# Optimization experiments

Hardware: AMD Instinct MI355X
Metric: run time of the kernel (lower is better)

Reference implementation:

```python
import jax, jax.numpy as jnp
import numpy as np

D_HEAD = 64
D_MODEL = 1024
N_HEADS = D_MODEL // D_HEAD
MAX_TOKENS = 2048


def setup_inputs() -> dict:
    key = jax.random.key(0)
    ks = jax.random.split(key, 5)
    batch, pos = 2, 2048
    # kaiming_normal_ on (n_heads, d_model, d_head): fan_in = d_model*d_head -> std = sqrt(2/fan_in)
    std_qkv = np.sqrt(2.0 / (D_MODEL * D_HEAD)).astype(np.float32)
    # xavier_normal_ on (d_model, d_model): std = sqrt(2/(fan_in+fan_out))
    std_out = np.sqrt(2.0 / (D_MODEL + D_MODEL)).astype(np.float32)
    return {
        "residual_stream": jax.random.normal(ks[0], (batch, pos, D_MODEL), dtype=jnp.float32),
        "weight_query": jax.random.normal(ks[1], (N_HEADS, D_MODEL, D_HEAD), dtype=jnp.float32) * std_qkv,
        "weight_key": jax.random.normal(ks[2], (N_HEADS, D_MODEL, D_HEAD), dtype=jnp.float32) * std_qkv,
        "weight_value": jax.random.normal(ks[3], (N_HEADS, D_MODEL, D_HEAD), dtype=jnp.float32) * std_qkv,
        "weight_out": jax.random.normal(ks[4], (D_MODEL, D_MODEL), dtype=jnp.float32) * std_out,
    }


def reference(residual_stream, weight_query, weight_key, weight_value, weight_out):
    # QKV projections: [b, p, m] x [h, m, d] -> [b, h, p, d]
    q = jnp.einsum('bpm,hmd->bhpd', residual_stream, weight_query)
    k = jnp.einsum('bpm,hmd->bhpd', residual_stream, weight_key)
    v = jnp.einsum('bpm,hmd->bhpd', residual_stream, weight_value)

    n_tokens = residual_stream.shape[1]
    # scaled scores [b, h, dest, src]
    scores = jnp.einsum('bhqd,bhkd->bhqk', q, k) / jnp.sqrt(jnp.float32(D_HEAD))
    # causal mask: -inf above the diagonal
    causal = jnp.tril(jnp.ones((n_tokens, n_tokens), dtype=bool))
    scores = jnp.where(causal, scores, jnp.float32(-jnp.inf))
    pattern = jax.nn.softmax(scores, axis=-1)

    attn = jnp.einsum('bhqk,bhkd->bhqd', pattern, v)  # [b, h, dest, d_head]
    # concat heads -> [b, p, h*d_head]
    b, h, p, d = attn.shape
    attn_concat = jnp.transpose(attn, (0, 2, 1, 3)).reshape(b, p, h * d)
    return jnp.einsum('bpm,mn->bpn', attn_concat, weight_out)
```

## Files before the change

### kernel.cpp

```cpp
#include <hip/hip_runtime.h>
#include <hip/hip_bf16.h>
#include <stdint.h>


typedef __bf16 bf16x8 __attribute__((ext_vector_type(8)));
typedef float f32x4 __attribute__((ext_vector_type(4)));
typedef unsigned short u16;

__device__ __forceinline__ u16 f2bf(float f) {
  unsigned u = __float_as_uint(f);
  u += 0x7fffu + ((u >> 16) & 1u);
  return (u16)(u >> 16);
}

__global__ __launch_bounds__(256) void xcvt_k(const float* __restrict__ in,
                                              u16* __restrict__ out) {
  int i = (blockIdx.x * 256 + threadIdx.x) * 8;
  float4 f0 = *reinterpret_cast<const float4*>(in + i);
  float4 f1 = *reinterpret_cast<const float4*>(in + i + 4);
  u16 tmp[8] = {f2bf(f0.x), f2bf(f0.y), f2bf(f0.z), f2bf(f0.w),
                f2bf(f1.x), f2bf(f1.y), f2bf(f1.z), f2bf(f1.w)};
  *reinterpret_cast<uint4*>(out + i) = *reinterpret_cast<uint4*>(tmp);
}

__global__ __launch_bounds__(256) void transpose_cvt_k(const float* __restrict__ in,
                                                       u16* __restrict__ out,
                                                       int R, int C) {
  __shared__ u16 tile[64][80];
  int b = blockIdx.z;
  int r0 = blockIdx.x * 64, c0 = blockIdx.y * 64;
  const float* ip = in + (size_t)b * R * C;
  u16* op = out + (size_t)b * R * C;
  int t = threadIdx.x;
  int r = t >> 2, cb = (t & 3) * 16;
  const float4* src = reinterpret_cast<const float4*>(ip + (size_t)(r0 + r) * C + c0 + cb);
  u16 tmp[16];
#pragma unroll
  for (int v = 0; v < 4; v++) {
    float4 f = src[v];
    tmp[v * 4 + 0] = f2bf(f.x);
    tmp[v * 4 + 1] = f2bf(f.y);
    tmp[v * 4 + 2] = f2bf(f.z);
    tmp[v * 4 + 3] = f2bf(f.w);
  }
  *reinterpret_cast<uint4*>(&tile[r][cb]) = *reinterpret_cast<uint4*>(&tmp[0]);
  *reinterpret_cast<uint4*>(&tile[r][cb + 8]) = *reinterpret_cast<uint4*>(&tmp[8]);
  __syncthreads();
  int c = t >> 2, rb = (t & 3) * 16;
  uint4 outv[2];
  u16* tp = reinterpret_cast<u16*>(outv);
#pragma unroll
  for (int j = 0; j < 16; j++) tp[j] = tile[rb + j][c];
  uint4* dst = reinterpret_cast<uint4*>(op + (size_t)(c0 + c) * R + r0 + rb);
  dst[0] = outv[0];
  dst[1] = outv[1];
}

__global__ __launch_bounds__(256) void transpose_qkv_k(const float* __restrict__ Wq,
                                                       const float* __restrict__ Wk,
                                                       const float* __restrict__ Wv,
                                                       u16* __restrict__ outBase) {
  __shared__ u16 tile[64][80];
  int z = blockIdx.z;
  int sel = z >> 4, head = z & 15;
  const float* W = (sel == 0) ? Wq : (sel == 1 ? Wk : Wv);
  const float* ip = W + (size_t)head * 65536;
  u16* op = outBase + (size_t)sel * 1048576 + (size_t)head * 65536;
  int r0 = blockIdx.x * 64;
  int t = threadIdx.x;
  int r = t >> 2, cb = (t & 3) * 16;
  const float4* src = reinterpret_cast<const float4*>(ip + (size_t)(r0 + r) * 64 + cb);
  u16 tmp[16];
#pragma unroll
  for (int v = 0; v < 4; v++) {
    float4 f = src[v];
    tmp[v * 4 + 0] = f2bf(f.x);
    tmp[v * 4 + 1] = f2bf(f.y);
    tmp[v * 4 + 2] = f2bf(f.z);
    tmp[v * 4 + 3] = f2bf(f.w);
  }
  *reinterpret_cast<uint4*>(&tile[r][cb]) = *reinterpret_cast<uint4*>(&tmp[0]);
  *reinterpret_cast<uint4*>(&tile[r][cb + 8]) = *reinterpret_cast<uint4*>(&tmp[8]);
  __syncthreads();
  int c = t >> 2, rb = (t & 3) * 16;
  uint4 outv[2];
  u16* tp = reinterpret_cast<u16*>(outv);
#pragma unroll
  for (int j = 0; j < 16; j++) tp[j] = tile[rb + j][c];
  uint4* dst = reinterpret_cast<uint4*>(op + (size_t)c * 1024 + r0 + rb);
  dst[0] = outv[0];
  dst[1] = outv[1];
}

__device__ __forceinline__ void gload16(const u16* g, u16* l) {
  __builtin_amdgcn_global_load_lds(
      (__attribute__((address_space(1))) void*)(g),
      (__attribute__((address_space(3))) void*)(l), 16, 0, 0);
}

__device__ __forceinline__ void gemm128_core(const u16* __restrict__ A,
                                             const u16* __restrict__ BT,
                                             int m0, int n0,
                                             f32x4 (&acc)[4][4]) {
  __shared__ __align__(16) u16 As[2][128][64];
  __shared__ __align__(16) u16 Bs[2][128][64];
  int t = threadIdx.x, l = t & 63;
  int w = t >> 6, wm = w & 1, wn = w >> 1;
  int l15 = l & 15, q4 = l >> 4;
  int r8 = l >> 3;
  int cs = ((l & 7) ^ r8) * 8;
  int swz = l15 & 7;
  int srow = w * 32 + r8;
  const u16* ga = A + (size_t)(m0 + srow) * 1024 + cs;
  const u16* gb = BT + (size_t)(n0 + srow) * 1024 + cs;
  f32x4 z4 = {0.f, 0.f, 0.f, 0.f};
#pragma unroll
  for (int mi = 0; mi < 4; mi++)
#pragma unroll
    for (int nt = 0; nt < 4; nt++) acc[mi][nt] = z4;

#pragma unroll
  for (int i = 0; i < 4; i++) {
    gload16(ga + (size_t)(i * 8) * 1024, &As[0][w * 32 + i * 8][0]);
    gload16(gb + (size_t)(i * 8) * 1024, &Bs[0][w * 32 + i * 8][0]);
  }
  __syncthreads();

  for (int step = 0; step < 16; step++) {
    int cur = step & 1;
    if (step < 15) {
      int k0 = (step + 1) * 64;
#pragma unroll
      for (int i = 0; i < 4; i++) {
        gload16(ga + (size_t)(i * 8) * 1024 + k0, &As[cur ^ 1][w * 32 + i * 8][0]);
        gload16(gb + (size_t)(i * 8) * 1024 + k0, &Bs[cur ^ 1][w * 32 + i * 8][0]);
      }
    }
#pragma unroll
    for (int kk = 0; kk < 2; kk++) {
      bf16x8 af[4], bfr[4];
#pragma unroll
      for (int mi = 0; mi < 4; mi++)
        af[mi] = *reinterpret_cast<const bf16x8*>(
            &As[cur][wm * 64 + mi * 16 + l15][((kk * 4 + q4) ^ swz) * 8]);
#pragma unroll
      for (int nt = 0; nt < 4; nt++)
        bfr[nt] = *reinterpret_cast<const bf16x8*>(
            &Bs[cur][wn * 64 + nt * 16 + l15][((kk * 4 + q4) ^ swz) * 8]);
#pragma unroll
      for (int mi = 0; mi < 4; mi++)
#pragma unroll
        for (int nt = 0; nt < 4; nt++)
          acc[mi][nt] = __builtin_amdgcn_mfma_f32_16x16x32_bf16(af[mi], bfr[nt], acc[mi][nt], 0, 0, 0);
    }
    __syncthreads();
  }
}

__global__ __launch_bounds__(256) void qkv_gemm128_k(const u16* __restrict__ A,
                                                     const u16* __restrict__ BT,
                                                     u16* __restrict__ Q,
                                                     u16* __restrict__ K,
                                                     u16* __restrict__ VT2) {
  const float QSCALE = 0.125f * 1.44269504088896340736f;
  int m0 = blockIdx.x * 128, n0 = blockIdx.y * 128;
  f32x4 acc[4][4];
  gemm128_core(A, BT, m0, n0, acc);
  int t = threadIdx.x, l = t & 63;
  int w = t >> 6, wm = w & 1, wn = w >> 1;
  int l15 = l & 15, q4 = l >> 4;
#pragma unroll
  for (int mi = 0; mi < 4; mi++) {
#pragma unroll
    for (int nt = 0; nt < 4; nt++) {
#pragma unroll
      for (int r = 0; r < 4; r++) {
        int m = m0 + wm * 64 + mi * 16 + q4 * 4 + r;
        int n = n0 + wn * 64 + nt * 16 + l15;
        int wsel = n >> 10, h = (n >> 6) & 15, d = n & 63;
        int b = m >> 11, p = m & 2047;
        size_t bh = (size_t)(b * 16 + h);
        float v = acc[mi][nt][r];
        if (wsel == 0)
          Q[(bh * 2048 + p) * 64 + d] = f2bf(v * QSCALE);
        else if (wsel == 1)
          K[(bh * 2048 + p) * 64 + d] = f2bf(v);
        else
          VT2[((bh * 32 + (p >> 6)) * 64 + d) * 64 + (p & 63)] = f2bf(v);
      }
    }
  }
}

__global__ __launch_bounds__(256) void out_gemm128_k(const u16* __restrict__ A,
                                                     const u16* __restrict__ BT,
                                                     float* __restrict__ O) {
  int m0 = blockIdx.x * 128, n0 = blockIdx.y * 128;
  f32x4 acc[4][4];
  gemm128_core(A, BT, m0, n0, acc);
  int t = threadIdx.x, l = t & 63;
  int w = t >> 6, wm = w & 1, wn = w >> 1;
  int l15 = l & 15, q4 = l >> 4;
#pragma unroll
  for (int mi = 0; mi < 4; mi++) {
#pragma unroll
    for (int nt = 0; nt < 4; nt++) {
#pragma unroll
      for (int r = 0; r < 4; r++) {
        int m = m0 + wm * 64 + mi * 16 + q4 * 4 + r;
        int n = n0 + wn * 64 + nt * 16 + l15;
        O[(size_t)m * 1024 + n] = acc[mi][nt][r];
      }
    }
  }
}

__global__ __launch_bounds__(256) void attn_k(const u16* __restrict__ Q,
                                              const u16* __restrict__ K,
                                              const u16* __restrict__ VT2,
                                              u16* __restrict__ A) {
  __shared__ __align__(16) u16 Ks[2][64][64];
  __shared__ __align__(16) u16 Vs[2][64][64];
  __shared__ u16 P[4][32][72];
  int pr = blockIdx.x, h = blockIdx.y, b = blockIdx.z;
  int qt = b ? (15 - pr) : pr;
  size_t bh = (size_t)(b * 16 + h);
  const u16* Qp = Q + bh * 2048 * 64;
  const u16* Kp = K + bh * 2048 * 64;
  const u16* Vt = VT2 + bh * 32 * 64 * 64;
  int t = threadIdx.x, l = t & 63, w = t >> 6;
  int l15 = l & 15, q4 = l >> 4;
  int r8 = l >> 3, cs = ((l & 7) ^ r8) * 8;
  int swz = l15 & 7;
  const float NEG = -1e30f;
  f32x4 z4 = {0.f, 0.f, 0.f, 0.f};
  int nkt = 2 * qt + 2;
  const u16* kbase = Kp + (size_t)(w * 16 + r8) * 64 + cs;
  const u16* vbase = Vt + (size_t)(w * 16 + r8) * 64 + cs;

  int qr0 = qt * 128 + w * 32;
  bf16x8 qf[2][2];
#pragma unroll
  for (int mi = 0; mi < 2; mi++) {
    const u16* qp = Qp + (size_t)(qr0 + mi * 16 + l15) * 64;
    qf[mi][0] = *reinterpret_cast<const bf16x8*>(qp + q4 * 8);
    qf[mi][1] = *reinterpret_cast<const bf16x8*>(qp + 32 + q4 * 8);
  }
  f32x4 accO[2][4];
  float rs[2][4];
#pragma unroll
  for (int mi = 0; mi < 2; mi++) {
#pragma unroll
    for (int nt = 0; nt < 4; nt++) accO[mi][nt] = z4;
#pragma unroll
    for (int r = 0; r < 4; r++) rs[mi][r] = 0.f;
  }

#pragma unroll
  for (int j = 0; j < 2; j++) {
    gload16(kbase + (size_t)(j * 512), &Ks[0][w * 16 + j * 8][0]);
    gload16(vbase + (size_t)(j * 512), &Vs[0][w * 16 + j * 8][0]);
  }
  __syncthreads();

  for (int kt = 0; kt < nkt; kt++) {
    int cur = kt & 1;
    if (kt < nkt - 1) {
      size_t off = (size_t)(kt + 1) * 4096;
#pragma unroll
      for (int j = 0; j < 2; j++) {
        gload16(kbase + off + j * 512, &Ks[cur ^ 1][w * 16 + j * 8][0]);
        gload16(vbase + off + j * 512, &Vs[cur ^ 1][w * 16 + j * 8][0]);
      }
    }

    f32x4 s[2][4];
#pragma unroll
    for (int mi = 0; mi < 2; mi++)
#pragma unroll
      for (int nt = 0; nt < 4; nt++) s[mi][nt] = z4;
    __builtin_amdgcn_s_setprio(1);
#pragma unroll
    for (int kk = 0; kk < 2; kk++) {
      bf16x8 kf[4];
#pragma unroll
      for (int nt = 0; nt < 4; nt++)
        kf[nt] = *reinterpret_cast<const bf16x8*>(
            &Ks[cur][nt * 16 + l15][((kk * 4 + q4) ^ swz) * 8]);
#pragma unroll
      for (int mi = 0; mi < 2; mi++)
#pragma unroll
        for (int nt = 0; nt < 4; nt++)
          s[mi][nt] = __builtin_amdgcn_mfma_f32_16x16x32_bf16(qf[mi][kk], kf[nt], s[mi][nt], 0, 0, 0);
    }
    __builtin_amdgcn_s_setprio(0);
    if (kt >= 2 * qt) {
      int colbase = (kt - 2 * qt) * 64;
      int rowl = w * 32 + q4 * 4;
#pragma unroll
      for (int mi = 0; mi < 2; mi++)
#pragma unroll
        for (int nt = 0; nt < 4; nt++)
#pragma unroll
          for (int r = 0; r < 4; r++)
            if (colbase + nt * 16 + l15 > rowl + mi * 16 + r) s[mi][nt][r] = NEG;
    }
#pragma unroll
    for (int mi = 0; mi < 2; mi++)
#pragma unroll
      for (int nt = 0; nt < 4; nt++)
#pragma unroll
        for (int r = 0; r < 4; r++) {
          float p = exp2f(s[mi][nt][r]);
          rs[mi][r] += p;
          P[w][mi * 16 + q4 * 4 + r][nt * 16 + l15] = f2bf(p);
        }
    __builtin_amdgcn_s_setprio(1);
#pragma unroll
    for (int kk = 0; kk < 2; kk++) {
      bf16x8 pa[2];
#pragma unroll
      for (int mi = 0; mi < 2; mi++)
        pa[mi] = *reinterpret_cast<const bf16x8*>(&P[w][mi * 16 + l15][kk * 32 + q4 * 8]);
#pragma unroll
      for (int nt = 0; nt < 4; nt++) {
        bf16x8 vf = *reinterpret_cast<const bf16x8*>(
            &Vs[cur][nt * 16 + l15][((kk * 4 + q4) ^ swz) * 8]);
#pragma unroll
        for (int mi = 0; mi < 2; mi++)
          accO[mi][nt] = __builtin_amdgcn_mfma_f32_16x16x32_bf16(pa[mi], vf, accO[mi][nt], 0, 0, 0);
      }
    }
    __builtin_amdgcn_s_setprio(0);
    __syncthreads();
  }

#pragma unroll
  for (int mi = 0; mi < 2; mi++)
#pragma unroll
    for (int r = 0; r < 4; r++) {
      float v = rs[mi][r];
#pragma unroll
      for (int sh = 1; sh < 16; sh <<= 1) v += __shfl_xor(v, sh, 64);
      float inv = 1.f / v;
      int prow = qt * 128 + w * 32 + mi * 16 + q4 * 4 + r;
      size_t base = ((size_t)(b * 2048 + prow)) * 1024 + h * 64;
#pragma unroll
      for (int nt = 0; nt < 4; nt++) A[base + nt * 16 + l15] = f2bf(accO[mi][nt][r] * inv);
    }
}

extern "C" void kernel_launch(void* const* d_in, const int* in_sizes, int n_in,
                              void* d_out, int out_size, void* d_ws, size_t ws_size,
                              hipStream_t stream) {
  const float* X  = (const float*)d_in[0];
  const float* Wq = (const float*)d_in[1];
  const float* Wk = (const float*)d_in[2];
  const float* Wv = (const float*)d_in[3];
  const float* Wo = (const float*)d_in[4];
  float* out = (float*)d_out;

  u16* ws = (u16*)d_ws;
  u16* WqT = ws;
  u16* WoT = WqT + 3145728;
  u16* Xb  = WoT + 1048576;
  u16* Qb  = Xb + 4194304;
  u16* Kb  = Qb + 4194304;
  u16* VT2 = Kb + 4194304;
  u16* Ab  = Xb;

  xcvt_k<<<dim3(2048), 256, 0, stream>>>(X, Xb);
  transpose_qkv_k<<<dim3(16, 1, 48), 256, 0, stream>>>(Wq, Wk, Wv, WqT);
  transpose_cvt_k<<<dim3(16, 16, 1), 256, 0, stream>>>(Wo, WoT, 1024, 1024);

  qkv_gemm128_k<<<dim3(32, 24), 256, 0, stream>>>(Xb, WqT, Qb, Kb, VT2);
  attn_k<<<dim3(16, 16, 2), 256, 0, stream>>>(Qb, Kb, VT2, Ab);
  out_gemm128_k<<<dim3(32, 8), 256, 0, stream>>>(Ab, WoT, out);
}
```

Measured before the change: 228.0 us.

## Switch attention to 32x32x16 MFMA with transposed scores and register-resident P

Rewrites the attention kernel to use 32x32x16 bf16 MFMA tiles, computing S^T (K as A operand, Q as B) so each lane owns one query row. The probabilities are packed to bf16 in registers with v_cvt_pk_bf16_f32 and redistributed across lane halves with v_permlane32_swap, which removes the per-wave P shared-memory staging and its LDS round trip. The row-sum reduction is simplified to one shuffle plus a small LDS buffer at the end. This relies on gfx950-specific instructions and the exact MFMA register layout; any layout mismatch would give wrong results.

```diff
diff --git a/kernel.cpp b/kernel.cpp
--- a/kernel.cpp
+++ b/kernel.cpp
@@ -5,12 +5,23 @@
 
 typedef __bf16 bf16x8 __attribute__((ext_vector_type(8)));
 typedef float f32x4 __attribute__((ext_vector_type(4)));
+typedef float f32x16 __attribute__((ext_vector_type(16)));
 typedef unsigned short u16;
 
 __device__ __forceinline__ u16 f2bf(float f) {
   unsigned u = __float_as_uint(f);
   u += 0x7fffu + ((u >> 16) & 1u);
   return (u16)(u >> 16);
+}
+
+__device__ __forceinline__ uint32_t cvtpk(float lo, float hi) {
+  uint32_t r;
+  asm("v_cvt_pk_bf16_f32 %0, %1, %2" : "=v"(r) : "v"(lo), "v"(hi));
+  return r;
+}
+
+__device__ __forceinline__ void pl32swap(uint32_t& a, uint32_t& b) {
+  asm volatile("v_permlane32_swap_b32 %0, %1" : "+v"(a), "+v"(b));
 }
 
 __global__ __launch_bounds__(256) void xcvt_k(const float* __restrict__ in,
@@ -221,7 +232,7 @@
                                               u16* __restrict__ A) {
   __shared__ __align__(16) u16 Ks[2][64][64];
   __shared__ __align__(16) u16 Vs[2][64][64];
-  __shared__ u16 P[4][32][72];
+  __shared__ float rsbuf[4][32];
   int pr = blockIdx.x, h = blockIdx.y, b = blockIdx.z;
   int qt = b ? (15 - pr) : pr;
   size_t bh = (size_t)(b * 16 + h);
@@ -229,32 +240,26 @@
   const u16* Kp = K + bh * 2048 * 64;
   const u16* Vt = VT2 + bh * 32 * 64 * 64;
   int t = threadIdx.x, l = t & 63, w = t >> 6;
-  int l15 = l & 15, q4 = l >> 4;
+  int l31 = l & 31, hi = l >> 5;
   int r8 = l >> 3, cs = ((l & 7) ^ r8) * 8;
-  int swz = l15 & 7;
+  int swz = l31 & 7;
   const float NEG = -1e30f;
-  f32x4 z4 = {0.f, 0.f, 0.f, 0.f};
   int nkt = 2 * qt + 2;
   const u16* kbase = Kp + (size_t)(w * 16 + r8) * 64 + cs;
   const u16* vbase = Vt + (size_t)(w * 16 + r8) * 64 + cs;
-
-  int qr0 = qt * 128 + w * 32;
-  bf16x8 qf[2][2];
-#pragma unroll
-  for (int mi = 0; mi < 2; mi++) {
-    const u16* qp = Qp + (size_t)(qr0 + mi * 16 + l15) * 64;
-    qf[mi][0] = *reinterpret_cast<const bf16x8*>(qp + q4 * 8);
-    qf[mi][1] = *reinterpret_cast<const bf16x8*>(qp + 32 + q4 * 8);
-  }
-  f32x4 accO[2][4];
-  float rs[2][4];
-#pragma unroll
-  for (int mi = 0; mi < 2; mi++) {
-#pragma unroll
-    for (int nt = 0; nt < 4; nt++) accO[mi][nt] = z4;
-#pragma unroll
-    for (int r = 0; r < 4; r++) rs[mi][r] = 0.f;
-  }
+  int qrow = qt * 128 + w * 32 + l31;
+
+  bf16x8 qb[4];
+#pragma unroll
+  for (int kc = 0; kc < 4; kc++)
+    qb[kc] = *reinterpret_cast<const bf16x8*>(Qp + (size_t)qrow * 64 + kc * 16 + hi * 8);
+
+  f32x16 accO[2];
+#pragma unroll
+  for (int dh = 0; dh < 2; dh++)
+#pragma unroll
+    for (int r = 0; r < 16; r++) accO[dh][r] = 0.f;
+  float rs = 0.f;
 
 #pragma unroll
   for (int j = 0; j < 2; j++) {
@@ -274,80 +279,83 @@
       }
     }
 
-    f32x4 s[2][4];
-#pragma unroll
-    for (int mi = 0; mi < 2; mi++)
-#pragma unroll
-      for (int nt = 0; nt < 4; nt++) s[mi][nt] = z4;
+    f32x16 st[2];
+#pragma unroll
+    for (int kvh = 0; kvh < 2; kvh++)
+#pragma unroll
+      for (int r = 0; r < 16; r++) st[kvh][r] = 0.f;
     __builtin_amdgcn_s_setprio(1);
 #pragma unroll
-    for (int kk = 0; kk < 2; kk++) {
-      bf16x8 kf[4];
-#pragma unroll
-      for (int nt = 0; nt < 4; nt++)
-        kf[nt] = *reinterpret_cast<const bf16x8*>(
-            &Ks[cur][nt * 16 + l15][((kk * 4 + q4) ^ swz) * 8]);
-#pragma unroll
-      for (int mi = 0; mi < 2; mi++)
-#pragma unroll
-        for (int nt = 0; nt < 4; nt++)
-          s[mi][nt] = __builtin_amdgcn_mfma_f32_16x16x32_bf16(qf[mi][kk], kf[nt], s[mi][nt], 0, 0, 0);
+    for (int kc = 0; kc < 4; kc++) {
+      bf16x8 ka0 = *reinterpret_cast<const bf16x8*>(
+          &Ks[cur][l31][((2 * kc + hi) ^ swz) * 8]);
+      bf16x8 ka1 = *reinterpret_cast<const bf16x8*>(
+          &Ks[cur][32 + l31][((2 * kc + hi) ^ swz) * 8]);
+      st[0] = __builtin_amdgcn_mfma_f32_32x32x16_bf16(ka0, qb[kc], st[0], 0, 0, 0);
+      st[1] = __builtin_amdgcn_mfma_f32_32x32x16_bf16(ka1, qb[kc], st[1], 0, 0, 0);
     }
     __builtin_amdgcn_s_setprio(0);
+
     if (kt >= 2 * qt) {
-      int colbase = (kt - 2 * qt) * 64;
-      int rowl = w * 32 + q4 * 4;
-#pragma unroll
-      for (int mi = 0; mi < 2; mi++)
-#pragma unroll
-        for (int nt = 0; nt < 4; nt++)
-#pragma unroll
-          for (int r = 0; r < 4; r++)
-            if (colbase + nt * 16 + l15 > rowl + mi * 16 + r) s[mi][nt][r] = NEG;
-    }
-#pragma unroll
-    for (int mi = 0; mi < 2; mi++)
-#pragma unroll
-      for (int nt = 0; nt < 4; nt++)
-#pragma unroll
-        for (int r = 0; r < 4; r++) {
-          float p = exp2f(s[mi][nt][r]);
-          rs[mi][r] += p;
-          P[w][mi * 16 + q4 * 4 + r][nt * 16 + l15] = f2bf(p);
+      int kvb = kt * 64;
+#pragma unroll
+      for (int kvh = 0; kvh < 2; kvh++)
+#pragma unroll
+        for (int r = 0; r < 16; r++) {
+          int kv = kvb + kvh * 32 + (r & 3) + 8 * (r >> 2) + 4 * hi;
+          if (kv > qrow) st[kvh][r] = NEG;
         }
+    }
+
+#pragma unroll
+    for (int kvh = 0; kvh < 2; kvh++)
+#pragma unroll
+      for (int r = 0; r < 16; r++) {
+        float p = exp2f(st[kvh][r]);
+        st[kvh][r] = p;
+        rs += p;
+      }
+
+    bf16x8 pa[4];
+#pragma unroll
+    for (int ks = 0; ks < 4; ks++) {
+      const f32x16& pp = st[ks >> 1];
+      const int s8 = (ks & 1) * 8;
+      uint32_t x0 = cvtpk(pp[s8 + 0], pp[s8 + 1]);
+      uint32_t x1 = cvtpk(pp[s8 + 2], pp[s8 + 3]);
+      uint32_t y0 = cvtpk(pp[s8 + 4], pp[s8 + 5]);
+      uint32_t y1 = cvtpk(pp[s8 + 6], pp[s8 + 7]);
+      pl32swap(x0, y0);
+      pl32swap(x1, y1);
+      uint32_t wds[4] = {x0, x1, y0, y1};
+      pa[ks] = *reinterpret_cast<const bf16x8*>(wds);
+    }
+
     __builtin_amdgcn_s_setprio(1);
 #pragma unroll
-    for (int kk = 0; kk < 2; kk++) {
-      bf16x8 pa[2];
-#pragma unroll
-      for (int mi = 0; mi < 2; mi++)
-        pa[mi] = *reinterpret_cast<const bf16x8*>(&P[w][mi * 16 + l15][kk * 32 + q4 * 8]);
-#pragma unroll
-      for (int nt = 0; nt < 4; nt++) {
-        bf16x8 vf = *reinterpret_cast<const bf16x8*>(
-            &Vs[cur][nt * 16 + l15][((kk * 4 + q4) ^ swz) * 8]);
-#pragma unroll
-        for (int mi = 0; mi < 2; mi++)
-          accO[mi][nt] = __builtin_amdgcn_mfma_f32_16x16x32_bf16(pa[mi], vf, accO[mi][nt], 0, 0, 0);
-      }
-    }
+    for (int dh = 0; dh < 2; dh++)
+#pragma unroll
+      for (int ks = 0; ks < 4; ks++) {
+        bf16x8 vb = *reinterpret_cast<const bf16x8*>(
+            &Vs[cur][dh * 32 + l31][((2 * ks + hi) ^ swz) * 8]);
+        accO[dh] = __builtin_amdgcn_mfma_f32_32x32x16_bf16(pa[ks], vb, accO[dh], 0, 0, 0);
+      }
     __builtin_amdgcn_s_setprio(0);
     __syncthreads();
   }
 
-#pragma unroll
-  for (int mi = 0; mi < 2; mi++)
-#pragma unroll
-    for (int r = 0; r < 4; r++) {
-      float v = rs[mi][r];
-#pragma unroll
-      for (int sh = 1; sh < 16; sh <<= 1) v += __shfl_xor(v, sh, 64);
-      float inv = 1.f / v;
-      int prow = qt * 128 + w * 32 + mi * 16 + q4 * 4 + r;
-      size_t base = ((size_t)(b * 2048 + prow)) * 1024 + h * 64;
-#pragma unroll
-      for (int nt = 0; nt < 4; nt++) A[base + nt * 16 + l15] = f2bf(accO[mi][nt][r] * inv);
-    }
+  rs += __shfl_xor(rs, 32, 64);
+  if (hi == 0) rsbuf[w][l31] = rs;
+  __syncthreads();
+#pragma unroll
+  for (int r = 0; r < 16; r++) {
+    int ql = (r & 3) + 8 * (r >> 2) + 4 * hi;
+    float inv = 1.f / rsbuf[w][ql];
+    int prow = qt * 128 + w * 32 + ql;
+    size_t base = ((size_t)(b * 2048 + prow)) * 1024 + h * 64;
+    A[base + l31] = f2bf(accO[0][r] * inv);
+    A[base + 32 + l31] = f2bf(accO[1][r] * inv);
+  }
 }
 
 extern "C" void kernel_launch(void* const* d_in, const int* in_sizes, int n_in,
```

Measured after the change: 217.2 us. 1.05x faster.
